# Kernel tuning notes

Hardware: AMD Instinct MI355X
Metric: run time of the kernel (lower is better)

The kernel has to match this reference:

```python
import jax, jax.numpy as jnp
import numpy as np

B, N, D = 64, 1024, 128
K = 6  # hardcoded neighbor count in the module


def setup_inputs() -> dict:
    key = jax.random.key(0)
    ks = jax.random.split(key, 11)
    def lin(k, out_d, in_d):
        kw, kb = jax.random.split(k)
        s = 1.0 / np.sqrt(in_d)
        W = jax.random.uniform(kw, (out_d, in_d), minval=-s, maxval=s, dtype=jnp.float32)
        b = jax.random.uniform(kb, (out_d,), minval=-s, maxval=s, dtype=jnp.float32)
        return W, b
    loc = jax.random.uniform(ks[0], (B, N, 2), dtype=jnp.float32)
    deadline = jax.random.uniform(ks[1], (B, N), dtype=jnp.float32)
    depot = jax.random.uniform(ks[2], (B, 2), dtype=jnp.float32)
    W3d, b3d = lin(ks[3], D, 3)
    W2d, b2d = lin(ks[4], D, 2)
    Wnb, bnb = lin(ks[5], D, K * D)
    Wdep, bdep = lin(ks[6], D, 2)
    return {"loc": loc, "deadline": deadline, "depot": depot,
            "W3d": W3d, "b3d": b3d, "W2d": W2d, "b2d": b2d,
            "Wnb": Wnb, "bnb": bnb, "Wdep": Wdep, "bdep": bdep}


def reference(loc, deadline, depot, W3d, b3d, W2d, b2d, Wnb, bnb, Wdep, bdep):
    x = jnp.concatenate([loc, deadline[:, :, None]], axis=2)  # [B,N,3]
    x2 = x[:, :, 0:2]                                          # [B,N,2]
    F2 = jnp.einsum('bnf,df->bnd', x2, W2d) + b2d              # [B,N,D]
    F3 = jnp.einsum('bnf,df->bnd', x, W3d) + b3d               # [B,N,D]
    # pairwise euclidean distances; indices are non-differentiable -> stop_gradient
    diff = x2[:, None, :, :] - x2[:, :, None, :]               # [B,N,N,2]
    dist = jnp.sqrt(jnp.sum(diff * diff, axis=-1))             # [B,N,N]
    _, neighbors = jax.lax.top_k(jax.lax.stop_gradient(-dist), K)  # [B,N,K] smallest dists (incl. self)
    # faithful quirk: original does F0_embedding_2d[:, neighbors][0] == gather from batch-0 embeddings
    nb = F2[0][neighbors]                                      # [B,N,K,D]
    nb_c = nb.reshape(nb.shape[0], nb.shape[1], K * nb.shape[3])  # [B,N,K*D]
    Fn = jnp.einsum('bnf,df->bnd', nb_c, Wnb) + bnb            # [B,N,D]
    Ff = Fn + F3
    dep = depot @ Wdep.T + bdep                                 # [B,D]
    h = jax.nn.leaky_relu(jnp.concatenate([dep[:, None, :], Ff], axis=1), negative_slope=0.01)
    return h, h.mean(axis=1)
```

## Files before the change

kernel.cpp:

```cpp
#include <hip/hip_runtime.h>
#include <hip/hip_bf16.h>

#define CB 64
#define CN 1024
#define CD 128
#define CK 6

typedef __attribute__((ext_vector_type(8))) short short8;
typedef __attribute__((ext_vector_type(4))) float floatx4;

__device__ __forceinline__ unsigned short f2bf(float f) {
    union { float f; unsigned u; } c; c.f = f;
    unsigned u = c.u;
    u += 0x7FFFu + ((u >> 16) & 1u);
    return (unsigned short)(u >> 16);
}

#define WS_G      0
#define WS_NBRS   3145728
#define WS_IDS    3932160
#define WS_STARTS 4063232
#define WS_BSUM   4129024
#define WS_CNT    4161792

struct SortSM { float2 pts[CN]; int cnt[256]; int base[256]; };
struct GSM    { unsigned short As[128 * 40]; unsigned short Bs[128 * 40]; };
union GridSM  { SortSM s; GSM g; };

__global__ void __launch_bounds__(256) k_gridg(
    const float* __restrict__ loc,
    const float* __restrict__ W2d,
    const float* __restrict__ b2d,
    const float* __restrict__ Wnb,
    unsigned short* __restrict__ ids,
    int* __restrict__ starts,
    float* __restrict__ G,
    float* __restrict__ bsum,
    int* __restrict__ cnt)
{
    __shared__ GridSM sm;
    int t = threadIdx.x;

    if (blockIdx.x < 64) {
        int b = blockIdx.x;
        if (t < 128) bsum[(b << 7) + t] = 0.f;
        if (t == 128) cnt[b] = 0;
        const float2* lb = (const float2*)loc + b * CN;
#pragma unroll
        for (int r = 0; r < 4; ++r) sm.s.pts[t + r * 256] = lb[t + r * 256];
        sm.s.cnt[t] = 0;
        __syncthreads();
        int mycell[4];
#pragma unroll
        for (int r = 0; r < 4; ++r) {
            float2 p = sm.s.pts[t * 4 + r];
            int cx = (int)(p.x * 16.0f); cx = cx > 15 ? 15 : cx;
            int cy = (int)(p.y * 16.0f); cy = cy > 15 ? 15 : cy;
            mycell[r] = (cy << 4) + cx;
            atomicAdd(&sm.s.cnt[mycell[r]], 1);
        }
        __syncthreads();
        for (int off = 1; off < 256; off <<= 1) {
            int u = (t >= off) ? sm.s.cnt[t - off] : 0;
            __syncthreads();
            sm.s.cnt[t] += u;
            __syncthreads();
        }
        int excl = (t == 0) ? 0 : sm.s.cnt[t - 1];
        sm.s.base[t] = excl;
        starts[b * 257 + t] = excl;
        if (t == 255) starts[b * 257 + 256] = sm.s.cnt[255];
        __syncthreads();
#pragma unroll
        for (int r = 0; r < 4; ++r) {
            int pos = atomicAdd(&sm.s.base[mycell[r]], 1);
            ids[b * CN + pos] = (unsigned short)(t * 4 + r);
        }
        return;
    }

    int gb = blockIdx.x - 64;
    int k = gb % 6;
    int tile = gb / 6;
    int n0 = tile << 7;

    int wave = t >> 6, lane = t & 63;
    int koff = (lane >> 4) * 8;
    int mrow = lane & 15;

    int e2 = t & 15, rg = t >> 4;
    float2 pl[8];
#pragma unroll
    for (int rr = 0; rr < 8; ++rr)
        pl[rr] = ((const float2*)loc)[n0 + rg + rr * 16];

    int bd = t >> 1, bhalf = t & 1;

    floatx4 acc[2][8];
#pragma unroll
    for (int i = 0; i < 2; ++i)
#pragma unroll
        for (int j = 0; j < 8; ++j) acc[i][j] = (floatx4){0.f, 0.f, 0.f, 0.f};

#pragma unroll
    for (int c = 0; c < 4; ++c) {
        __syncthreads();
        {
            int e0 = c * 32 + e2 * 2;
            float wx0 = W2d[e0 * 2],     wy0 = W2d[e0 * 2 + 1], bz0 = b2d[e0];
            float wx1 = W2d[e0 * 2 + 2], wy1 = W2d[e0 * 2 + 3], bz1 = b2d[e0 + 1];
#pragma unroll
            for (int rr = 0; rr < 8; ++rr) {
                float2 p = pl[rr];
                float v0 = fmaf(p.x, wx0, fmaf(p.y, wy0, bz0));
                float v1 = fmaf(p.x, wx1, fmaf(p.y, wy1, bz1));
                unsigned pack = (unsigned)f2bf(v0) | ((unsigned)f2bf(v1) << 16);
                *(unsigned*)&sm.g.As[(rg + rr * 16) * 40 + e2 * 2] = pack;
            }
        }
        {
            const float* src = Wnb + bd * 768 + k * 128 + c * 32 + bhalf * 16;
            float4 f0 = *(const float4*)(src);
            float4 f1 = *(const float4*)(src + 4);
            float4 f2v = *(const float4*)(src + 8);
            float4 f3 = *(const float4*)(src + 12);
            uint4 o0, o1;
            o0.x = (unsigned)f2bf(f0.x) | ((unsigned)f2bf(f0.y) << 16);
            o0.y = (unsigned)f2bf(f0.z) | ((unsigned)f2bf(f0.w) << 16);
            o0.z = (unsigned)f2bf(f1.x) | ((unsigned)f2bf(f1.y) << 16);
            o0.w = (unsigned)f2bf(f1.z) | ((unsigned)f2bf(f1.w) << 16);
            o1.x = (unsigned)f2bf(f2v.x) | ((unsigned)f2bf(f2v.y) << 16);
            o1.y = (unsigned)f2bf(f2v.z) | ((unsigned)f2bf(f2v.w) << 16);
            o1.z = (unsigned)f2bf(f3.x) | ((unsigned)f2bf(f3.y) << 16);
            o1.w = (unsigned)f2bf(f3.z) | ((unsigned)f2bf(f3.w) << 16);
            *(uint4*)&sm.g.Bs[bd * 40 + bhalf * 16] = o0;
            *(uint4*)&sm.g.Bs[bd * 40 + bhalf * 16 + 8] = o1;
        }
        __syncthreads();
        short8 af[2];
#pragma unroll
        for (int i = 0; i < 2; ++i)
            af[i] = *(const short8*)&sm.g.As[(wave * 32 + i * 16 + mrow) * 40 + koff];
#pragma unroll
        for (int j = 0; j < 8; ++j) {
            short8 bfr = *(const short8*)&sm.g.Bs[(j * 16 + mrow) * 40 + koff];
#pragma unroll
            for (int i = 0; i < 2; ++i)
                acc[i][j] = __builtin_amdgcn_mfma_f32_16x16x32_bf16(
                    af[i], bfr, acc[i][j], 0, 0, 0);
        }
    }

    int lq = lane >> 4, lc = lane & 15;
#pragma unroll
    for (int j = 0; j < 8; ++j) {
        int d = j * 16 + lc;
#pragma unroll
        for (int i = 0; i < 2; ++i) {
#pragma unroll
            for (int r = 0; r < 4; ++r) {
                int row = wave * 32 + i * 16 + lq * 4 + r;
                G[(n0 + row) * 768 + k * 128 + d] = acc[i][j][r];
            }
        }
    }
}

__global__ void __launch_bounds__(256) k_knn(
    const float* __restrict__ loc,
    const unsigned short* __restrict__ ids,
    const int* __restrict__ starts,
    unsigned short* __restrict__ nbrs)
{
    __shared__ float2 xy_tmp[CN];
    __shared__ float2 xy_s[CN];
    __shared__ unsigned short ids_s[CN];
    __shared__ int st_s[257];
    int t = threadIdx.x;
    int b = blockIdx.x >> 4;
    int qbase = (blockIdx.x & 15) << 6;
    const float2* lb = (const float2*)loc + b * CN;
#pragma unroll
    for (int r = 0; r < 4; ++r) {
        int p = t + r * 256;
        xy_tmp[p] = lb[p];
        ids_s[p] = ids[b * CN + p];
    }
    st_s[t] = starts[b * 257 + t];
    if (t == 0) st_s[256] = starts[b * 257 + 256];
    __syncthreads();
#pragma unroll
    for (int r = 0; r < 4; ++r) {
        int p = t + r * 256;
        xy_s[p] = xy_tmp[ids_s[p]];
    }
    __syncthreads();

    int qp = qbase + (t >> 2);
    int pi = t & 3;
    int q = ids_s[qp];
    float2 qxy = xy_s[qp];
    float xq = qxy.x, yq = qxy.y;
    int cx = (int)(xq * 16.0f); cx = cx > 15 ? 15 : cx;
    int cy = (int)(yq * 16.0f); cy = cy > 15 ? 15 : cy;
    float dk[CK]; int ik[CK];
#pragma unroll
    for (int s = 0; s < CK; ++s) { dk[s] = 1e30f; ik[s] = 0x7FFFFFFF; }
    float dk5sq = __builtin_inff();
    const float h = 0.0625f;

#define KNN_CAND(P)                                                        \
    {                                                                      \
        float2 v = xy_s[P];                                                \
        float dx = __fsub_rn(v.x, xq);                                     \
        float dy = __fsub_rn(v.y, yq);                                     \
        float d2 = __fadd_rn(__fmul_rn(dx, dx), __fmul_rn(dy, dy));        \
        if (d2 < dk5sq) {                                                  \
            float ds = __fsqrt_rn(d2);                                     \
            int j = ids_s[P];                                              \
            if (ds < dk[CK - 1] || (ds == dk[CK - 1] && j < ik[CK - 1])) { \
                float dc = ds; int jc = j;                                 \
                _Pragma("unroll")                                          \
                for (int s = 0; s < CK; ++s) {                             \
                    bool sw = (dc < dk[s]) || (dc == dk[s] && jc < ik[s]); \
                    float od = dk[s]; int oi = ik[s];                      \
                    dk[s] = sw ? dc : od; ik[s] = sw ? jc : oi;            \
                    dc = sw ? od : dc;    jc = sw ? oi : jc;               \
                }                                                          \
                if (ik[CK - 1] != 0x7FFFFFFF)                              \
                    dk5sq = __fmul_rn(dk[CK - 1], dk[CK - 1]) * 1.000001f; \
            }                                                              \
        }                                                                  \
    }

#define KNN_MERGE(MASK)                                                     \
    {                                                                       \
        float od[CK]; int oi[CK];                                           \
        _Pragma("unroll")                                                   \
        for (int s = 0; s < CK; ++s) {                                      \
            od[s] = __shfl_xor(dk[s], MASK);                                \
            oi[s] = __shfl_xor(ik[s], MASK);                                \
        }                                                                   \
        _Pragma("unroll")                                                   \
        for (int e = 0; e < CK; ++e) {                                      \
            float dc = od[e]; int jc = oi[e];                               \
            if ((dc < dk[CK - 1]) || (dc == dk[CK - 1] && jc < ik[CK - 1])) { \
                _Pragma("unroll")                                           \
                for (int s = 0; s < CK; ++s) {                              \
                    bool sw = (dc < dk[s]) || (dc == dk[s] && jc < ik[s]);  \
                    float td = dk[s]; int ti = ik[s];                       \
                    dk[s] = sw ? dc : td; ik[s] = sw ? jc : ti;             \
                    dc = sw ? td : dc;    jc = sw ? ti : jc;                \
                }                                                           \
            }                                                               \
        }                                                                   \
    }

#define KNN_MERGE_D(MASK)                                                   \
    {                                                                       \
        float od[CK]; int oi[CK];                                           \
        _Pragma("unroll")                                                   \
        for (int s = 0; s < CK; ++s) {                                      \
            od[s] = __shfl_xor(dk[s], MASK);                                \
            oi[s] = __shfl_xor(ik[s], MASK);                                \
        }                                                                   \
        _Pragma("unroll")                                                   \
        for (int e = 0; e < CK; ++e) {                                      \
            float dc = od[e]; int jc = oi[e];                               \
            bool dup = false;                                               \
            _Pragma("unroll")                                               \
            for (int s = 0; s < CK; ++s) dup = dup || (jc == ik[s]);        \
            if (!dup &&                                                     \
                ((dc < dk[CK - 1]) || (dc == dk[CK - 1] && jc < ik[CK - 1]))) { \
                _Pragma("unroll")                                           \
                for (int s = 0; s < CK; ++s) {                              \
                    bool sw = (dc < dk[s]) || (dc == dk[s] && jc < ik[s]);  \
                    float td = dk[s]; int ti = ik[s];                       \
                    dk[s] = sw ? dc : td; ik[s] = sw ? jc : ti;             \
                    dc = sw ? td : dc;    jc = sw ? ti : jc;                \
                }                                                           \
            }                                                               \
        }                                                                   \
    }

    {
        int yl = cy > 0 ? cy - 1 : 0, yh = cy < 15 ? cy + 1 : 15;
        int xl = cx > 0 ? cx - 1 : 0, xh = cx < 15 ? cx + 1 : 15;
        for (int yy = yl; yy <= yh; ++yy) {
            int p  = st_s[(yy << 4) + xl] + pi;
            int pe = st_s[(yy << 4) + xh + 1];
            for (; p < pe; p += 4) KNN_CAND(p)
        }
    }

    KNN_MERGE(1)
    KNN_MERGE(2)

    bool done;
    {
        int x0 = cx - 1, x1 = cx + 1, y0 = cy - 1, y1 = cy + 1;
        done = (x0 <= 0 && y0 <= 0 && x1 >= 15 && y1 >= 15);
        float mL = x0 > 0  ? __fsub_rn(xq, (float)x0 * h)       : 1e30f;
        float mR = x1 < 15 ? __fsub_rn((float)(x1 + 1) * h, xq) : 1e30f;
        float mB = y0 > 0  ? __fsub_rn(yq, (float)y0 * h)       : 1e30f;
        float mT = y1 < 15 ? __fsub_rn((float)(y1 + 1) * h, yq) : 1e30f;
        float bound = fminf(fminf(mL, mR), fminf(mB, mT)) * 0.999999f;
        done = done || (ik[CK - 1] != 0x7FFFFFFF && dk[CK - 1] < bound);
    }

    if (__any(!done)) {
        if (!done) {
            if (ik[CK - 1] != 0x7FFFFFFF)
                dk5sq = __fmul_rn(dk[CK - 1], dk[CK - 1]) * 1.000001f;
            for (int r = 2; r < 16; ++r) {
                int x0 = cx - r, x1 = cx + r, y0 = cy - r, y1 = cy + r;
                int yl = y0 < 0 ? 0 : y0, yh = y1 > 15 ? 15 : y1;
                int xl = x0 < 0 ? 0 : x0, xh = x1 > 15 ? 15 : x1;
                for (int yy = yl; yy <= yh; ++yy) {
                    bool ey = (yy == y0) || (yy == y1);
                    if (ey) {
                        int p  = st_s[(yy << 4) + xl] + pi;
                        int pe = st_s[(yy << 4) + xh + 1];
                        for (; p < pe; p += 4) KNN_CAND(p)
                    } else {
                        if (x0 >= 0) {
                            int p  = st_s[(yy << 4) + x0] + pi;
                            int pe = st_s[(yy << 4) + x0 + 1];
                            for (; p < pe; p += 4) KNN_CAND(p)
                        }
                        if (x1 <= 15) {
                            int p  = st_s[(yy << 4) + x1] + pi;
                            int pe = st_s[(yy << 4) + x1 + 1];
                            for (; p < pe; p += 4) KNN_CAND(p)
                        }
                    }
                }
                if (x0 <= 0 && y0 <= 0 && x1 >= 15 && y1 >= 15) break;
                float mL = x0 > 0  ? __fsub_rn(xq, (float)x0 * h)       : 1e30f;
                float mR = x1 < 15 ? __fsub_rn((float)(x1 + 1) * h, xq) : 1e30f;
                float mB = y0 > 0  ? __fsub_rn(yq, (float)y0 * h)       : 1e30f;
                float mT = y1 < 15 ? __fsub_rn((float)(y1 + 1) * h, yq) : 1e30f;
                float bound = fminf(fminf(mL, mR), fminf(mB, mT)) * 0.999999f;
                if (ik[CK - 1] != 0x7FFFFFFF && dk[CK - 1] < bound) break;
            }
        }
        KNN_MERGE_D(1)
        KNN_MERGE_D(2)
    }
#undef KNN_CAND
#undef KNN_MERGE
#undef KNN_MERGE_D

    if (pi == 0) {
        unsigned short* o = nbrs + (unsigned)(b * CN + q) * CK;
#pragma unroll
        for (int s = 0; s < CK; ++s) o[s] = (unsigned short)ik[s];
    }
}

__global__ void __launch_bounds__(256) k_gatherfin(
    const float* __restrict__ loc,
    const float* __restrict__ dl,
    const unsigned short* __restrict__ nbrs,
    const float* __restrict__ G,
    const float* __restrict__ W3d,
    const float* __restrict__ b3d,
    const float* __restrict__ bnb,
    const float* __restrict__ depot,
    const float* __restrict__ Wdep,
    const float* __restrict__ bdep,
    float* __restrict__ out,
    float* __restrict__ bsum,
    int* __restrict__ cnt)
{
    __shared__ float psum[4][CD];
    __shared__ unsigned short nbs[64 * CK];
    __shared__ int lastflag;
    int t = threadIdx.x, bx = blockIdx.x;
    int rowbase = bx << 6, b = rowbase >> 10;

    if (t < 192)
        ((unsigned*)nbs)[t] = ((const unsigned*)(nbrs + (size_t)rowbase * CK))[t];

    int d4 = t & 31, rg = t >> 5;
    int d0 = d4 * 4;
    float4 w0, w1, w2, bias;
#pragma unroll
    for (int dd = 0; dd < 4; ++dd) {
        int d = d0 + dd;
        ((float*)&w0)[dd] = W3d[d * 3];
        ((float*)&w1)[dd] = W3d[d * 3 + 1];
        ((float*)&w2)[dd] = W3d[d * 3 + 2];
        ((float*)&bias)[dd] = b3d[d] + bnb[d];
    }
    float4 csum = {0.f, 0.f, 0.f, 0.f};
    __syncthreads();

    for (int rr = 0; rr < 8; ++rr) {
        int r = rr * 8 + rg;
        int gr = rowbase + r;
        const unsigned short* nb = nbs + r * CK;
        float4 a = {0.f, 0.f, 0.f, 0.f};
#pragma unroll
        for (int k2 = 0; k2 < CK; ++k2) {
            int m = nb[k2];
            float4 g4 = *(const float4*)(G + m * 768 + k2 * 128 + d0);
            a.x += g4.x; a.y += g4.y; a.z += g4.z; a.w += g4.w;
        }
        float2 l2 = ((const float2*)loc)[gr];
        float dlv = dl[gr];
        float4 v;
        v.x = a.x + bias.x + l2.x * w0.x + l2.y * w1.x + dlv * w2.x;
        v.y = a.y + bias.y + l2.x * w0.y + l2.y * w1.y + dlv * w2.y;
        v.z = a.z + bias.z + l2.x * w0.z + l2.y * w1.z + dlv * w2.z;
        v.w = a.w + bias.w + l2.x * w0.w + l2.y * w1.w + dlv * w2.w;
        float4 lr;
        lr.x = v.x >= 0.f ? v.x : 0.01f * v.x;
        lr.y = v.y >= 0.f ? v.y : 0.01f * v.y;
        lr.z = v.z >= 0.f ? v.z : 0.01f * v.z;
        lr.w = v.w >= 0.f ? v.w : 0.01f * v.w;
        *(float4*)(out + ((long)b * 1025 + (gr & 1023) + 1) * 128 + d0) = lr;
        csum.x += lr.x; csum.y += lr.y; csum.z += lr.z; csum.w += lr.w;
    }

    csum.x += __shfl_xor(csum.x, 32);
    csum.y += __shfl_xor(csum.y, 32);
    csum.z += __shfl_xor(csum.z, 32);
    csum.w += __shfl_xor(csum.w, 32);
    int wave = t >> 6, lane = t & 63;
    if (lane < 32) *(float4*)&psum[wave][d0] = csum;
    __syncthreads();
    if (t < CD)
        atomicAdd(bsum + (b << 7) + t,
                  psum[0][t] + psum[1][t] + psum[2][t] + psum[3][t]);
    __syncthreads();
    if (t == 0) {
        __threadfence();
        int old = atomicAdd(cnt + b, 1);
        lastflag = (old == 15);
    }
    __syncthreads();
    if (lastflag && t < CD) {
        float acc = atomicAdd(bsum + (b << 7) + t, 0.0f);
        float dv = depot[b * 2] * Wdep[t * 2] + depot[b * 2 + 1] * Wdep[t * 2 + 1]
                 + bdep[t];
        float lr = dv >= 0.f ? dv : 0.01f * dv;
        out[(long)b * 1025 * 128 + t] = lr;
        out[(long)CB * 1025 * 128 + (b << 7) + t] =
            (acc + lr) * (1.0f / 1025.0f);
    }
}

extern "C" void kernel_launch(void* const* d_in, const int* in_sizes, int n_in,
                              void* d_out, int out_size, void* d_ws, size_t ws_size,
                              hipStream_t stream) {
    const float* loc      = (const float*)d_in[0];
    const float* deadline = (const float*)d_in[1];
    const float* depot    = (const float*)d_in[2];
    const float* W3d      = (const float*)d_in[3];
    const float* b3d      = (const float*)d_in[4];
    const float* W2d      = (const float*)d_in[5];
    const float* b2d      = (const float*)d_in[6];
    const float* Wnb      = (const float*)d_in[7];
    const float* bnb      = (const float*)d_in[8];
    const float* Wdep     = (const float*)d_in[9];
    const float* bdep     = (const float*)d_in[10];
    float* out = (float*)d_out;

    char* ws = (char*)d_ws;
    float* G              = (float*)(ws + WS_G);
    unsigned short* nbrs  = (unsigned short*)(ws + WS_NBRS);
    unsigned short* ids   = (unsigned short*)(ws + WS_IDS);
    int* starts           = (int*)(ws + WS_STARTS);
    float* bsum           = (float*)(ws + WS_BSUM);
    int* cnt              = (int*)(ws + WS_CNT);

    k_gridg<<<112, 256, 0, stream>>>(loc, W2d, b2d, Wnb, ids, starts, G,
                                     bsum, cnt);
    k_knn<<<1024, 256, 0, stream>>>(loc, ids, starts, nbrs);
    k_gatherfin<<<1024, 256, 0, stream>>>(loc, deadline, nbrs, G, W3d, b3d,
                                          bnb, depot, Wdep, bdep, out,
                                          bsum, cnt);
}
```

Before: 152.7 us.

## Double-buffer neighbor gathers, halve rows per block, use nontemporal output stores

The gather-finalize kernel now handles 32 rows per block across 2048 blocks instead of 64 rows across 1024, which doubles the number of blocks and the batch-completion count threshold. The row loop is unrolled into a two-stage software pipeline, so the six G loads for the next row are issued before the current row is reduced, which hides gather latency. Output writes use nontemporal stores to avoid cache pollution. The cost is more registers and twice as many atomics on the per-batch sums and counters.

```diff
diff --git a/kernel.cpp b/kernel.cpp
--- a/kernel.cpp
+++ b/kernel.cpp
@@ -374,12 +374,12 @@
     int* __restrict__ cnt)
 {
     __shared__ float psum[4][CD];
-    __shared__ unsigned short nbs[64 * CK];
+    __shared__ unsigned short nbs[32 * CK];
     __shared__ int lastflag;
     int t = threadIdx.x, bx = blockIdx.x;
-    int rowbase = bx << 6, b = rowbase >> 10;
-
-    if (t < 192)
+    int rowbase = bx << 5, b = bx >> 5;
+
+    if (t < 96)
         ((unsigned*)nbs)[t] = ((const unsigned*)(nbrs + (size_t)rowbase * CK))[t];
 
     int d4 = t & 31, rg = t >> 5;
@@ -396,39 +396,69 @@
     float4 csum = {0.f, 0.f, 0.f, 0.f};
     __syncthreads();
 
-    for (int rr = 0; rr < 8; ++rr) {
-        int r = rr * 8 + rg;
-        int gr = rowbase + r;
-        const unsigned short* nb = nbs + r * CK;
-        float4 a = {0.f, 0.f, 0.f, 0.f};
-#pragma unroll
-        for (int k2 = 0; k2 < CK; ++k2) {
-            int m = nb[k2];
-            float4 g4 = *(const float4*)(G + m * 768 + k2 * 128 + d0);
-            a.x += g4.x; a.y += g4.y; a.z += g4.z; a.w += g4.w;
-        }
-        float2 l2 = ((const float2*)loc)[gr];
-        float dlv = dl[gr];
-        float4 v;
-        v.x = a.x + bias.x + l2.x * w0.x + l2.y * w1.x + dlv * w2.x;
-        v.y = a.y + bias.y + l2.x * w0.y + l2.y * w1.y + dlv * w2.y;
-        v.z = a.z + bias.z + l2.x * w0.z + l2.y * w1.z + dlv * w2.z;
-        v.w = a.w + bias.w + l2.x * w0.w + l2.y * w1.w + dlv * w2.w;
-        float4 lr;
-        lr.x = v.x >= 0.f ? v.x : 0.01f * v.x;
-        lr.y = v.y >= 0.f ? v.y : 0.01f * v.y;
-        lr.z = v.z >= 0.f ? v.z : 0.01f * v.z;
-        lr.w = v.w >= 0.f ? v.w : 0.01f * v.w;
-        *(float4*)(out + ((long)b * 1025 + (gr & 1023) + 1) * 128 + d0) = lr;
-        csum.x += lr.x; csum.y += lr.y; csum.z += lr.z; csum.w += lr.w;
-    }
+    float4 gA[6], gB[6];
+    float2 lA, lB; float dA, dB;
+
+#define GISSUE(RR, S)                                                       \
+    {                                                                       \
+        int r = (RR) * 8 + rg;                                              \
+        const unsigned short* nb = nbs + r * CK;                            \
+        g##S[0] = *(const float4*)(G + nb[0] * 768 + 0 * 128 + d0);         \
+        g##S[1] = *(const float4*)(G + nb[1] * 768 + 1 * 128 + d0);         \
+        g##S[2] = *(const float4*)(G + nb[2] * 768 + 2 * 128 + d0);         \
+        g##S[3] = *(const float4*)(G + nb[3] * 768 + 3 * 128 + d0);         \
+        g##S[4] = *(const float4*)(G + nb[4] * 768 + 4 * 128 + d0);         \
+        g##S[5] = *(const float4*)(G + nb[5] * 768 + 5 * 128 + d0);         \
+        l##S = ((const float2*)loc)[rowbase + r];                           \
+        d##S = dl[rowbase + r];                                             \
+    }
+
+#define GCONSUME(RR, S)                                                     \
+    {                                                                       \
+        int r = (RR) * 8 + rg;                                              \
+        int gr = rowbase + r;                                               \
+        float4 a;                                                           \
+        a.x = ((((g##S[0].x + g##S[1].x) + g##S[2].x) + g##S[3].x) + g##S[4].x) + g##S[5].x; \
+        a.y = ((((g##S[0].y + g##S[1].y) + g##S[2].y) + g##S[3].y) + g##S[4].y) + g##S[5].y; \
+        a.z = ((((g##S[0].z + g##S[1].z) + g##S[2].z) + g##S[3].z) + g##S[4].z) + g##S[5].z; \
+        a.w = ((((g##S[0].w + g##S[1].w) + g##S[2].w) + g##S[3].w) + g##S[4].w) + g##S[5].w; \
+        float4 v;                                                           \
+        v.x = a.x + bias.x + l##S.x * w0.x + l##S.y * w1.x + d##S * w2.x;   \
+        v.y = a.y + bias.y + l##S.x * w0.y + l##S.y * w1.y + d##S * w2.y;   \
+        v.z = a.z + bias.z + l##S.x * w0.z + l##S.y * w1.z + d##S * w2.z;   \
+        v.w = a.w + bias.w + l##S.x * w0.w + l##S.y * w1.w + d##S * w2.w;   \
+        floatx4 lr;                                                         \
+        lr.x = v.x >= 0.f ? v.x : 0.01f * v.x;                              \
+        lr.y = v.y >= 0.f ? v.y : 0.01f * v.y;                              \
+        lr.z = v.z >= 0.f ? v.z : 0.01f * v.z;                              \
+        lr.w = v.w >= 0.f ? v.w : 0.01f * v.w;                              \
+        __builtin_nontemporal_store(lr,                                     \
+            (floatx4*)(out + ((long)b * 1025 + (gr & 1023) + 1) * 128 + d0));\
+        csum.x += lr.x; csum.y += lr.y; csum.z += lr.z; csum.w += lr.w;     \
+    }
+
+    GISSUE(0, A)
+    GISSUE(1, B)
+    GCONSUME(0, A)
+    GISSUE(2, A)
+    GCONSUME(1, B)
+    GISSUE(3, B)
+    GCONSUME(2, A)
+    GCONSUME(3, B)
+#undef GISSUE
+#undef GCONSUME
 
     csum.x += __shfl_xor(csum.x, 32);
     csum.y += __shfl_xor(csum.y, 32);
     csum.z += __shfl_xor(csum.z, 32);
     csum.w += __shfl_xor(csum.w, 32);
     int wave = t >> 6, lane = t & 63;
-    if (lane < 32) *(float4*)&psum[wave][d0] = csum;
+    if (lane < 32) {
+        psum[wave][d0]     = csum.x;
+        psum[wave][d0 + 1] = csum.y;
+        psum[wave][d0 + 2] = csum.z;
+        psum[wave][d0 + 3] = csum.w;
+    }
     __syncthreads();
     if (t < CD)
         atomicAdd(bsum + (b << 7) + t,
@@ -437,7 +467,7 @@
     if (t == 0) {
         __threadfence();
         int old = atomicAdd(cnt + b, 1);
-        lastflag = (old == 15);
+        lastflag = (old == 31);
     }
     __syncthreads();
     if (lastflag && t < CD) {
@@ -478,7 +508,7 @@
     k_gridg<<<112, 256, 0, stream>>>(loc, W2d, b2d, Wnb, ids, starts, G,
                                      bsum, cnt);
     k_knn<<<1024, 256, 0, stream>>>(loc, ids, starts, nbrs);
-    k_gatherfin<<<1024, 256, 0, stream>>>(loc, deadline, nbrs, G, W3d, b3d,
+    k_gatherfin<<<2048, 256, 0, stream>>>(loc, deadline, nbrs, G, W3d, b3d,
                                           bnb, depot, Wdep, bdep, out,
                                           bsum, cnt);
 }
```

New measurement: 189.9 us. +24.4%, slower.
